# Optimization experiments

Measured on AMD Instinct MI355X. Metric: run time of the kernel, lower is better.

Reference implementation:

```python
import jax, jax.numpy as jnp
import numpy as np
import math

D_KEY = 64
D_VALUE = 64
NUM_HEADS = 16
D_MODEL = D_VALUE * NUM_HEADS  # 1024


def setup_inputs() -> dict:
    key = jax.random.key(0)
    ks = jax.random.split(key, 5)
    B, N = 2, 2048
    s = 1.0 / math.sqrt(D_MODEL)
    return {
        "x": jax.random.normal(ks[0], (B, N, D_MODEL), dtype=jnp.float32),
        "Wq": jax.random.normal(ks[1], (D_MODEL, D_KEY * NUM_HEADS), dtype=jnp.float32) * s,
        "Wk": jax.random.normal(ks[2], (D_MODEL, D_KEY * NUM_HEADS), dtype=jnp.float32) * s,
        "Wv": jax.random.normal(ks[3], (D_MODEL, D_MODEL), dtype=jnp.float32) * s,
        "Wp": jax.random.normal(ks[4], (D_MODEL, D_MODEL), dtype=jnp.float32) * s,
    }


def reference(x, Wq, Wk, Wv, Wp):
    # x: [B, N, d_model]. Equivalent to the original block-diagonal concat trick:
    # off-diagonal blocks are -inf, so softmax over the key axis reduces to
    # independent per-head softmax attention.
    B, N, D = x.shape
    H, K, V = NUM_HEADS, D_KEY, D_VALUE
    scale = 1.0 / math.sqrt(K)
    q = (x @ Wq).reshape(B, N, H, K)
    k = (x @ Wk).reshape(B, N, H, K)
    v = (x @ Wv).reshape(B, N, H, V)
    scores = jnp.einsum("bnhk,bmhk->bhnm", q, k) * scale  # [B,H,N,N]
    attn = jax.nn.softmax(scores, axis=-1)
    out = jnp.einsum("bhnm,bmhv->bnhv", attn, v).reshape(B, N, D)
    return x + out @ Wp
```

## Files before the change

### kernel.cpp

```cpp
#include <hip/hip_runtime.h>

typedef float f32x4 __attribute__((ext_vector_type(4)));
typedef __bf16 bf16x8 __attribute__((ext_vector_type(8)));

#define DEV static __device__ __forceinline__

DEV ushort f2bf(float f) {
  unsigned u = __builtin_bit_cast(unsigned, f);
  u += 0x7FFFu + ((u >> 16) & 1u);
  return (ushort)(u >> 16);
}

DEV bf16x8 ld_frag(const ushort* p) {
  return __builtin_bit_cast(bf16x8, *reinterpret_cast<const int4*>(p));
}

DEV bf16x8 ld_lds(const ushort* base, int byte_off) {
  return __builtin_bit_cast(bf16x8,
      *reinterpret_cast<const int4*>(reinterpret_cast<const char*>(base) + byte_off));
}

DEV int swz(int row, int col_byte) { return row * 128 + (col_byte ^ ((row & 7) << 4)); }

DEV float fast_exp2(float x) {
  float r;
  asm("v_exp_f32 %0, %1" : "=v"(r) : "v"(x));
  return r;
}

DEV unsigned cvt_pk_bf16(float lo, float hi) {
  unsigned r;
  asm("v_cvt_pk_bf16_f32 %0, %1, %2" : "=v"(r) : "v"(lo), "v"(hi));
  return r;
}

DEV void gload16(const ushort* g, ushort* l) {
  __builtin_amdgcn_global_load_lds(
      (const __attribute__((address_space(1))) unsigned int*)g,
      (__attribute__((address_space(3))) unsigned int*)l, 16, 0, 0);
}


__global__ __launch_bounds__(256) void convert_x(const float* __restrict__ x,
                                                 ushort* __restrict__ xb) {
  int i = blockIdx.x * 256 + threadIdx.x;
  float4 v = reinterpret_cast<const float4*>(x)[i];
  ushort4 o = make_ushort4(f2bf(v.x), f2bf(v.y), f2bf(v.z), f2bf(v.w));
  reinterpret_cast<ushort4*>(xb)[i] = o;
}

__global__ __launch_bounds__(256) void transpose_w(const float* __restrict__ w0,
                                                   const float* __restrict__ w1,
                                                   const float* __restrict__ w2,
                                                   const float* __restrict__ w3,
                                                   ushort* __restrict__ wt) {
  __shared__ float tile[32][33];
  const int z = blockIdx.z;
  const float* w = z == 0 ? w0 : z == 1 ? w1 : z == 2 ? w2 : w3;
  ushort* out = wt + (size_t)z * 1024 * 1024;
  const int n0 = blockIdx.x * 32, k0 = blockIdx.y * 32;
  const int tx = threadIdx.x, ty = threadIdx.y;
#pragma unroll
  for (int i = 0; i < 4; ++i)
    tile[ty + i * 8][tx] = w[(size_t)(k0 + ty + i * 8) * 1024 + n0 + tx];
  __syncthreads();
#pragma unroll
  for (int i = 0; i < 4; ++i)
    out[(size_t)(n0 + ty + i * 8) * 1024 + k0 + tx] = f2bf(tile[tx][ty + i * 8]);
}


DEV void gemm_core(const ushort* __restrict__ A, const ushort* __restrict__ BT,
                   ushort* a_lds, ushort* b_lds, int row0, int col0, f32x4 acc[4][4]) {
  const int tid = threadIdx.x;
  const int lane = tid & 63;
  const int w = tid >> 6, wr = w >> 1, wc = w & 1;
  const int lg = lane >> 4, l15 = lane & 15;
  const int srow = w * 32 + (lane >> 3);
  const int scol = ((lane & 7) ^ (lane >> 3)) << 3;
  const ushort* ga = A + (size_t)(row0 + srow) * 1024 + scol;
  const ushort* gb = BT + (size_t)(col0 + srow) * 1024 + scol;
#pragma unroll
  for (int ai = 0; ai < 4; ++ai)
#pragma unroll
    for (int bj = 0; bj < 4; ++bj) acc[ai][bj] = f32x4{0.f, 0.f, 0.f, 0.f};

  for (int kt = 0; kt < 1024; kt += 64) {
    __syncthreads();
#pragma unroll
    for (int p = 0; p < 4; ++p) {
      gload16(ga + kt + (size_t)(p * 8) * 1024, a_lds + (w * 32 + p * 8) * 64);
      gload16(gb + kt + (size_t)(p * 8) * 1024, b_lds + (w * 32 + p * 8) * 64);
    }
    __syncthreads();
    bf16x8 af[4][2], bfr[4][2];
#pragma unroll
    for (int i = 0; i < 4; ++i)
#pragma unroll
      for (int kk = 0; kk < 2; ++kk) {
        af[i][kk] = ld_lds(a_lds, swz(wr * 64 + i * 16 + l15, kk * 64 + lg * 16));
        bfr[i][kk] = ld_lds(b_lds, swz(wc * 64 + i * 16 + l15, kk * 64 + lg * 16));
      }
#pragma unroll
    for (int kk = 0; kk < 2; ++kk)
#pragma unroll
      for (int ai = 0; ai < 4; ++ai)
#pragma unroll
        for (int bj = 0; bj < 4; ++bj)
          acc[ai][bj] = __builtin_amdgcn_mfma_f32_16x16x32_bf16(af[ai][kk], bfr[bj][kk],
                                                                acc[ai][bj], 0, 0, 0);
  }
}

__global__ __launch_bounds__(256) void gemm_qkv(const ushort* __restrict__ xb,
                                                const ushort* __restrict__ wqT,
                                                const ushort* __restrict__ wkT,
                                                const ushort* __restrict__ wvT,
                                                ushort* __restrict__ q, ushort* __restrict__ k,
                                                ushort* __restrict__ vt) {
  __shared__ ushort a_lds[128 * 64], b_lds[128 * 64];
  const int fid = blockIdx.x;
  const int wid = (fid & 7) * 96 + (fid >> 3);
  const int row = wid / 24, rem = wid % 24;
  const int col = rem / 3, z = rem % 3;
  const int row0 = row * 128, col0 = col * 128;
  const ushort* BT = z == 0 ? wqT : z == 1 ? wkT : wvT;
  f32x4 acc[4][4];
  gemm_core(xb, BT, a_lds, b_lds, row0, col0, acc);
  const int lane = threadIdx.x & 63;
  const int w = threadIdx.x >> 6, wr = w >> 1, wc = w & 1;
  const int lg = lane >> 4, l15 = lane & 15;
  if (z < 2) {
    ushort* out = z == 0 ? q : k;
    const float sc = z == 0 ? 0.125f * 1.4426950408889634f : 1.0f;
#pragma unroll
    for (int ai = 0; ai < 4; ++ai)
#pragma unroll
      for (int bj = 0; bj < 4; ++bj)
#pragma unroll
        for (int r = 0; r < 4; ++r) {
          int orow = row0 + wr * 64 + ai * 16 + lg * 4 + r;
          int ocol = col0 + wc * 64 + bj * 16 + l15;
          out[(size_t)orow * 1024 + ocol] = f2bf(acc[ai][bj][r] * sc);
        }
  } else {
#pragma unroll
    for (int ai = 0; ai < 4; ++ai)
#pragma unroll
      for (int bj = 0; bj < 4; ++bj) {
        int orow = row0 + wr * 64 + ai * 16 + lg * 4;
        int ocol = col0 + wc * 64 + bj * 16 + l15;
        int bb = orow >> 11, n = orow & 2047;
        ushort4 pk = make_ushort4(f2bf(acc[ai][bj][0]), f2bf(acc[ai][bj][1]),
                                  f2bf(acc[ai][bj][2]), f2bf(acc[ai][bj][3]));
        *reinterpret_cast<ushort4*>(vt + ((size_t)(bb * 1024 + ocol)) * 2048 + n) = pk;
      }
  }
}

__global__ __launch_bounds__(256) void gemm_out(const ushort* __restrict__ ob,
                                                const ushort* __restrict__ wpT,
                                                const float* __restrict__ x,
                                                float* __restrict__ y) {
  __shared__ ushort a_lds[128 * 64], b_lds[64 * 64];
  const int fid = blockIdx.x;
  const int wid = (fid & 7) * 64 + (fid >> 3);
  const int row0 = (wid >> 4) * 128, col0 = (wid & 15) * 64;
  const int tid = threadIdx.x;
  const int lane = tid & 63;
  const int w = tid >> 6, wr = w >> 1, wc = w & 1;
  const int lg = lane >> 4, l15 = lane & 15;
  const int sr8 = lane >> 3;
  const int scol = ((lane & 7) ^ sr8) << 3;
  const ushort* ga = ob + (size_t)(row0 + w * 32 + sr8) * 1024 + scol;
  const ushort* gb = wpT + (size_t)(col0 + w * 16 + sr8) * 1024 + scol;

  f32x4 acc[4][2];
#pragma unroll
  for (int ai = 0; ai < 4; ++ai)
#pragma unroll
    for (int bj = 0; bj < 2; ++bj) acc[ai][bj] = f32x4{0.f, 0.f, 0.f, 0.f};

  for (int kt = 0; kt < 1024; kt += 64) {
    __syncthreads();
#pragma unroll
    for (int p = 0; p < 4; ++p)
      gload16(ga + kt + (size_t)(p * 8) * 1024, a_lds + (w * 32 + p * 8) * 64);
#pragma unroll
    for (int p = 0; p < 2; ++p)
      gload16(gb + kt + (size_t)(p * 8) * 1024, b_lds + (w * 16 + p * 8) * 64);
    __syncthreads();
    bf16x8 af[4][2], bfr[2][2];
#pragma unroll
    for (int kk = 0; kk < 2; ++kk) {
#pragma unroll
      for (int i = 0; i < 4; ++i)
        af[i][kk] = ld_lds(a_lds, swz(wr * 64 + i * 16 + l15, kk * 64 + lg * 16));
#pragma unroll
      for (int j = 0; j < 2; ++j)
        bfr[j][kk] = ld_lds(b_lds, swz(wc * 32 + j * 16 + l15, kk * 64 + lg * 16));
    }
#pragma unroll
    for (int kk = 0; kk < 2; ++kk)
#pragma unroll
      for (int ai = 0; ai < 4; ++ai)
#pragma unroll
        for (int bj = 0; bj < 2; ++bj)
          acc[ai][bj] = __builtin_amdgcn_mfma_f32_16x16x32_bf16(af[ai][kk], bfr[bj][kk],
                                                                acc[ai][bj], 0, 0, 0);
  }

#pragma unroll
  for (int ai = 0; ai < 4; ++ai)
#pragma unroll
    for (int bj = 0; bj < 2; ++bj)
#pragma unroll
      for (int r = 0; r < 4; ++r) {
        int orow = row0 + wr * 64 + ai * 16 + lg * 4 + r;
        int ocol = col0 + wc * 32 + bj * 16 + l15;
        size_t idx = (size_t)orow * 1024 + ocol;
        y[idx] = x[idx] + acc[ai][bj][r];
      }
}

__global__ __launch_bounds__(256) void attn(const ushort* __restrict__ qg,
                                            const ushort* __restrict__ kg,
                                            const ushort* __restrict__ vtg,
                                            ushort* __restrict__ og) {
  __shared__ ushort k_lds[4 * 64 * 64];
  __shared__ ushort v_lds[4 * 64 * 64];
  const int fid = blockIdx.x;
  const int wid = (fid & 7) * 64 + (fid >> 3);
  const int bh = wid >> 4, q0 = wid & 15;
  const int b = bh >> 4, h = bh & 15;
  const int n0 = q0 * 128;
  const int tid = threadIdx.x, lane = tid & 63, w = tid >> 6;
  const int lg = lane >> 4, l15 = lane & 15;

  bf16x8 qf[2][2];
#pragma unroll
  for (int qi = 0; qi < 2; ++qi)
#pragma unroll
    for (int d32 = 0; d32 < 2; ++d32)
      qf[qi][d32] = ld_frag(qg + (size_t)(b * 2048 + n0 + w * 32 + qi * 16 + l15) * 1024 +
                            h * 64 + d32 * 32 + lg * 8);

  f32x4 o[2][4];
#pragma unroll
  for (int qi = 0; qi < 2; ++qi)
#pragma unroll
    for (int bj = 0; bj < 4; ++bj) o[qi][bj] = f32x4{0.f, 0.f, 0.f, 0.f};
  f32x4 ssum[2] = {f32x4{0.f, 0.f, 0.f, 0.f}, f32x4{0.f, 0.f, 0.f, 0.f}};

  const int sr8 = lane >> 3;
  const int scol = ((lane & 7) ^ sr8) << 3;
  const ushort* kbase = kg + (size_t)(b * 2048 + w * 16 + sr8) * 1024 + h * 64 + scol;
  const ushort* vbase = vtg + (size_t)(b * 1024 + h * 64 + w * 16 + sr8) * 2048 + scol;

  auto stage_sub = [&](ushort* kdst, ushort* vdst, int kv0) {
#pragma unroll
    for (int p = 0; p < 2; ++p) {
      gload16(kbase + (size_t)(kv0 + p * 8) * 1024, kdst + (w * 16 + p * 8) * 64);
      gload16(vbase + (size_t)(p * 8) * 2048 + kv0, vdst + (w * 16 + p * 8) * 64);
    }
  };
  auto stage2 = [&](int buf, int kv0) {
    stage_sub(k_lds + (2 * buf) * 4096, v_lds + (2 * buf) * 4096, kv0);
    stage_sub(k_lds + (2 * buf + 1) * 4096, v_lds + (2 * buf + 1) * 4096, kv0 + 64);
  };

  const int4 ones4 = make_int4(0x3F803F80, 0x3F803F80, 0x3F803F80, 0x3F803F80);
  const bf16x8 onesf = __builtin_bit_cast(bf16x8, ones4);

  auto qk_sub = [&](const ushort* kb, f32x4 s[2][4]) {
#pragma unroll
    for (int qi = 0; qi < 2; ++qi)
#pragma unroll
      for (int kj = 0; kj < 4; ++kj) s[qi][kj] = f32x4{0.f, 0.f, 0.f, 0.f};
#pragma unroll
    for (int d32 = 0; d32 < 2; ++d32)
#pragma unroll
      for (int kj = 0; kj < 4; ++kj) {
        bf16x8 kf = ld_lds(kb, swz(kj * 16 + l15, d32 * 64 + lg * 16));
        s[0][kj] = __builtin_amdgcn_mfma_f32_16x16x32_bf16(kf, qf[0][d32], s[0][kj], 0, 0, 0);
        s[1][kj] = __builtin_amdgcn_mfma_f32_16x16x32_bf16(kf, qf[1][d32], s[1][kj], 0, 0, 0);
      }
  };

  auto sm_pv_sub = [&](const ushort* vb, f32x4 s[2][4]) {
    bf16x8 pa[2][2];
#pragma unroll
    for (int qi = 0; qi < 2; ++qi) {
      unsigned pk[4][2];
#pragma unroll
      for (int kj = 0; kj < 4; ++kj) {
        float p0 = fast_exp2(s[qi][kj][0]);
        float p1 = fast_exp2(s[qi][kj][1]);
        float p2 = fast_exp2(s[qi][kj][2]);
        float p3 = fast_exp2(s[qi][kj][3]);
        pk[kj][0] = cvt_pk_bf16(p0, p1);
        pk[kj][1] = cvt_pk_bf16(p2, p3);
      }
#pragma unroll
      for (int k32 = 0; k32 < 2; ++k32) {
        unsigned x0 = pk[2 * k32][0], y0 = pk[2 * k32 + 1][0];
        unsigned x1 = pk[2 * k32][1], y1 = pk[2 * k32 + 1][1];
        asm("v_permlane32_swap_b32 %0, %1" : "+v"(x0), "+v"(y0));
        asm("v_permlane32_swap_b32 %0, %1" : "+v"(x1), "+v"(y1));
        asm("v_permlane16_swap_b32 %0, %1" : "+v"(x0), "+v"(y0));
        asm("v_permlane16_swap_b32 %0, %1" : "+v"(x1), "+v"(y1));
        int4 fr = make_int4(x0, x1, y0, y1);
        pa[qi][k32] = __builtin_bit_cast(bf16x8, fr);
      }
    }
#pragma unroll
    for (int qi = 0; qi < 2; ++qi) {
      ssum[qi] = __builtin_amdgcn_mfma_f32_16x16x32_bf16(pa[qi][0], onesf, ssum[qi], 0, 0, 0);
      ssum[qi] = __builtin_amdgcn_mfma_f32_16x16x32_bf16(pa[qi][1], onesf, ssum[qi], 0, 0, 0);
    }
#pragma unroll
    for (int k32 = 0; k32 < 2; ++k32)
#pragma unroll
      for (int bj = 0; bj < 4; ++bj) {
        bf16x8 vf = ld_lds(vb, swz(bj * 16 + l15, k32 * 64 + lg * 16));
        o[0][bj] = __builtin_amdgcn_mfma_f32_16x16x32_bf16(pa[0][k32], vf, o[0][bj], 0, 0, 0);
        o[1][bj] = __builtin_amdgcn_mfma_f32_16x16x32_bf16(pa[1][k32], vf, o[1][bj], 0, 0, 0);
      }
  };

  auto body2 = [&](int buf) {
    const ushort* kb0 = k_lds + (2 * buf) * 4096;
    const ushort* kb1 = k_lds + (2 * buf + 1) * 4096;
    const ushort* vb0 = v_lds + (2 * buf) * 4096;
    const ushort* vb1 = v_lds + (2 * buf + 1) * 4096;
    f32x4 s0[2][4], s1[2][4];
    qk_sub(kb0, s0);
    qk_sub(kb1, s1);
    sm_pv_sub(vb0, s0);
    sm_pv_sub(vb1, s1);
  };

  stage2(0, 0);
  __syncthreads();

  for (int tt = 0; tt < 8; ++tt) {
    stage2(1, (2 * tt + 1) * 128);
    body2(0);
    __syncthreads();
    if (tt < 7) stage2(0, (2 * tt + 2) * 128);
    body2(1);
    __syncthreads();
  }

#pragma unroll
  for (int qi = 0; qi < 2; ++qi) {
    f32x4 inv;
#pragma unroll
    for (int r = 0; r < 4; ++r) inv[r] = 1.0f / ssum[qi][r];
#pragma unroll
    for (int bj = 0; bj < 4; ++bj)
#pragma unroll
      for (int r = 0; r < 4; ++r) {
        int n = n0 + w * 32 + qi * 16 + lg * 4 + r;
        og[(size_t)(b * 2048 + n) * 1024 + h * 64 + bj * 16 + l15] = f2bf(o[qi][bj][r] * inv[r]);
      }
  }
}


extern "C" void kernel_launch(void* const* d_in, const int* in_sizes, int n_in,
                              void* d_out, int out_size, void* d_ws, size_t ws_size,
                              hipStream_t stream) {
  const float* x = (const float*)d_in[0];
  const float* Wq = (const float*)d_in[1];
  const float* Wk = (const float*)d_in[2];
  const float* Wv = (const float*)d_in[3];
  const float* Wp = (const float*)d_in[4];
  float* y = (float*)d_out;

  char* ws = (char*)d_ws;
  ushort* xb = (ushort*)(ws);
  ushort* wT = (ushort*)(ws + (8ull << 20));
  ushort* qw = (ushort*)(ws + (16ull << 20));
  ushort* kw = (ushort*)(ws + (24ull << 20));
  ushort* vtw = (ushort*)(ws + (32ull << 20));
  ushort* ow = (ushort*)(ws);

  convert_x<<<4096, 256, 0, stream>>>(x, xb);
  transpose_w<<<dim3(32, 32, 4), dim3(32, 8), 0, stream>>>(Wq, Wk, Wv, Wp, wT);
  gemm_qkv<<<768, 256, 0, stream>>>(xb, wT, wT + (1u << 20), wT + (2u << 20), qw, kw, vtw);
  attn<<<512, 256, 0, stream>>>(qw, kw, vtw, ow);
  gemm_out<<<512, 256, 0, stream>>>(ow, wT + (3u << 20), x, y);
}
```

Before: 114.8 us.

## Load K/V fragments directly from global into registers, drop LDS staging

Removes the shared-memory double buffer for K and V tiles in the attention kernel and loads the MFMA operand fragments straight from global memory into registers, using register double-buffering for K and a single prefetched V buffer. This removes LDS writes, swizzled LDS reads and all block-wide barriers. In exchange, each of the four waves now fetches the same K/V data independently, which raises global/L2 traffic fourfold. It also adds register pressure and exposes load latency, since the V loads are issued right before they are consumed.

```diff
diff --git a/kernel.cpp b/kernel.cpp
--- a/kernel.cpp
+++ b/kernel.cpp
@@ -227,8 +227,6 @@
                                             const ushort* __restrict__ kg,
                                             const ushort* __restrict__ vtg,
                                             ushort* __restrict__ og) {
-  __shared__ ushort k_lds[4 * 64 * 64];
-  __shared__ ushort v_lds[4 * 64 * 64];
   const int fid = blockIdx.x;
   const int wid = (fid & 7) * 64 + (fid >> 3);
   const int bh = wid >> 4, q0 = wid & 15;
@@ -252,27 +250,28 @@
     for (int bj = 0; bj < 4; ++bj) o[qi][bj] = f32x4{0.f, 0.f, 0.f, 0.f};
   f32x4 ssum[2] = {f32x4{0.f, 0.f, 0.f, 0.f}, f32x4{0.f, 0.f, 0.f, 0.f}};
 
-  const int sr8 = lane >> 3;
-  const int scol = ((lane & 7) ^ sr8) << 3;
-  const ushort* kbase = kg + (size_t)(b * 2048 + w * 16 + sr8) * 1024 + h * 64 + scol;
-  const ushort* vbase = vtg + (size_t)(b * 1024 + h * 64 + w * 16 + sr8) * 2048 + scol;
-
-  auto stage_sub = [&](ushort* kdst, ushort* vdst, int kv0) {
-#pragma unroll
-    for (int p = 0; p < 2; ++p) {
-      gload16(kbase + (size_t)(kv0 + p * 8) * 1024, kdst + (w * 16 + p * 8) * 64);
-      gload16(vbase + (size_t)(p * 8) * 2048 + kv0, vdst + (w * 16 + p * 8) * 64);
-    }
+  const ushort* kp = kg + (size_t)(b * 2048 + l15) * 1024 + h * 64 + lg * 8;
+  const ushort* vp = vtg + (size_t)(b * 1024 + h * 64 + l15) * 2048 + lg * 8;
+
+  auto load_k = [&](bf16x8 kr[4][2], int kv0) {
+#pragma unroll
+    for (int kj = 0; kj < 4; ++kj)
+#pragma unroll
+      for (int d32 = 0; d32 < 2; ++d32)
+        kr[kj][d32] = ld_frag(kp + (size_t)(kv0 + kj * 16) * 1024 + d32 * 32);
   };
-  auto stage2 = [&](int buf, int kv0) {
-    stage_sub(k_lds + (2 * buf) * 4096, v_lds + (2 * buf) * 4096, kv0);
-    stage_sub(k_lds + (2 * buf + 1) * 4096, v_lds + (2 * buf + 1) * 4096, kv0 + 64);
+  auto load_v = [&](bf16x8 vr[4][2], int kv0) {
+#pragma unroll
+    for (int bj = 0; bj < 4; ++bj)
+#pragma unroll
+      for (int k32 = 0; k32 < 2; ++k32)
+        vr[bj][k32] = ld_frag(vp + (size_t)(bj * 16) * 2048 + kv0 + k32 * 32);
   };
 
   const int4 ones4 = make_int4(0x3F803F80, 0x3F803F80, 0x3F803F80, 0x3F803F80);
   const bf16x8 onesf = __builtin_bit_cast(bf16x8, ones4);
 
-  auto qk_sub = [&](const ushort* kb, f32x4 s[2][4]) {
+  auto qk_sub = [&](const bf16x8 kr[4][2], f32x4 s[2][4]) {
 #pragma unroll
     for (int qi = 0; qi < 2; ++qi)
 #pragma unroll
@@ -281,13 +280,12 @@
     for (int d32 = 0; d32 < 2; ++d32)
 #pragma unroll
       for (int kj = 0; kj < 4; ++kj) {
-        bf16x8 kf = ld_lds(kb, swz(kj * 16 + l15, d32 * 64 + lg * 16));
-        s[0][kj] = __builtin_amdgcn_mfma_f32_16x16x32_bf16(kf, qf[0][d32], s[0][kj], 0, 0, 0);
-        s[1][kj] = __builtin_amdgcn_mfma_f32_16x16x32_bf16(kf, qf[1][d32], s[1][kj], 0, 0, 0);
+        s[0][kj] = __builtin_amdgcn_mfma_f32_16x16x32_bf16(kr[kj][d32], qf[0][d32], s[0][kj], 0, 0, 0);
+        s[1][kj] = __builtin_amdgcn_mfma_f32_16x16x32_bf16(kr[kj][d32], qf[1][d32], s[1][kj], 0, 0, 0);
       }
   };
 
-  auto sm_pv_sub = [&](const ushort* vb, f32x4 s[2][4]) {
+  auto sm_pv = [&](const bf16x8 vr[4][2], f32x4 s[2][4]) {
     bf16x8 pa[2][2];
 #pragma unroll
     for (int qi = 0; qi < 2; ++qi) {
@@ -322,34 +320,31 @@
     for (int k32 = 0; k32 < 2; ++k32)
 #pragma unroll
       for (int bj = 0; bj < 4; ++bj) {
-        bf16x8 vf = ld_lds(vb, swz(bj * 16 + l15, k32 * 64 + lg * 16));
-        o[0][bj] = __builtin_amdgcn_mfma_f32_16x16x32_bf16(pa[0][k32], vf, o[0][bj], 0, 0, 0);
-        o[1][bj] = __builtin_amdgcn_mfma_f32_16x16x32_bf16(pa[1][k32], vf, o[1][bj], 0, 0, 0);
+        o[0][bj] = __builtin_amdgcn_mfma_f32_16x16x32_bf16(pa[0][k32], vr[bj][k32], o[0][bj], 0, 0, 0);
+        o[1][bj] = __builtin_amdgcn_mfma_f32_16x16x32_bf16(pa[1][k32], vr[bj][k32], o[1][bj], 0, 0, 0);
       }
   };
 
-  auto body2 = [&](int buf) {
-    const ushort* kb0 = k_lds + (2 * buf) * 4096;
-    const ushort* kb1 = k_lds + (2 * buf + 1) * 4096;
-    const ushort* vb0 = v_lds + (2 * buf) * 4096;
-    const ushort* vb1 = v_lds + (2 * buf + 1) * 4096;
-    f32x4 s0[2][4], s1[2][4];
-    qk_sub(kb0, s0);
-    qk_sub(kb1, s1);
-    sm_pv_sub(vb0, s0);
-    sm_pv_sub(vb1, s1);
-  };
-
-  stage2(0, 0);
-  __syncthreads();
-
-  for (int tt = 0; tt < 8; ++tt) {
-    stage2(1, (2 * tt + 1) * 128);
-    body2(0);
-    __syncthreads();
-    if (tt < 7) stage2(0, (2 * tt + 2) * 128);
-    body2(1);
-    __syncthreads();
+  bf16x8 kA[4][2], kB[4][2], vA[4][2];
+  load_k(kA, 0);
+  load_k(kB, 64);
+  load_v(vA, 0);
+
+  for (int t = 0; t < 32; t += 2) {
+    {
+      f32x4 s[2][4];
+      qk_sub(kA, s);
+      if (t + 2 < 32) load_k(kA, (t + 2) * 64);
+      sm_pv(vA, s);
+      load_v(vA, (t + 1) * 64);
+    }
+    {
+      f32x4 s[2][4];
+      qk_sub(kB, s);
+      if (t + 3 < 32) load_k(kB, (t + 3) * 64);
+      sm_pv(vA, s);
+      if (t + 2 < 32) load_v(vA, (t + 2) * 64);
+    }
   }
 
 #pragma unroll
```

Result: slower. 191.8 us (+67.1%).
